# Kernel tuning notes

Measured on AMD Instinct MI355X. Metric: run time of the kernel, lower is better.

Reference implementation:

```python
import jax, jax.numpy as jnp
import numpy as np

N = 262144          # number of coordinate points
IN = 3              # coordinate dim
FF = 256            # fourier feature dim (out_features)
NFREQ = FF // 2     # 128 frequencies
H = 256             # mlp hidden width
L = 4               # hidden sine layers
OUT = 2             # Fullmodel hard-codes out_features=2 for the MLP
OMEGA0 = 30.0


def setup_inputs() -> dict:
    key = jax.random.key(0)
    ks = jax.random.split(key, 12)
    x = jax.random.normal(ks[0], (N, IN), dtype=jnp.float32)
    # Fourier encoder params (non-trainable in torch, still float inputs here)
    scales = jnp.ones((1, IN), dtype=jnp.float32)  # coordinate_scales = [1,1,1]
    B = jax.random.normal(ks[1], (IN, NFREQ), dtype=jnp.float32) * 3.0 * 10.0  # N(0,3)*10
    # SIREN first layer: uniform(-1/in, 1/in), in = FF
    W0 = jax.random.uniform(ks[2], (H, FF), dtype=jnp.float32, minval=-1.0 / FF, maxval=1.0 / FF)
    b0 = jax.random.uniform(ks[3], (H,), dtype=jnp.float32, minval=-1.0 / np.sqrt(FF), maxval=1.0 / np.sqrt(FF))
    # Hidden sine layers: uniform(-sqrt(6/in), sqrt(6/in)), in = H
    c = float(np.sqrt(6.0 / H))
    Wh = jax.random.uniform(ks[4], (L, H, H), dtype=jnp.float32, minval=-c, maxval=c)
    bh = jax.random.uniform(ks[5], (L, H), dtype=jnp.float32, minval=-1.0 / np.sqrt(H), maxval=1.0 / np.sqrt(H))
    # Final plain linear H -> OUT (default torch init, any small values fine)
    Wf = jax.random.uniform(ks[6], (OUT, H), dtype=jnp.float32, minval=-1.0 / np.sqrt(H), maxval=1.0 / np.sqrt(H))
    bf = jax.random.uniform(ks[7], (OUT,), dtype=jnp.float32, minval=-1.0 / np.sqrt(H), maxval=1.0 / np.sqrt(H))
    return {"x": x, "scales": scales, "B": B, "W0": W0, "b0": b0,
            "Wh": Wh, "bh": bh, "Wf": Wf, "bf": bf}


def reference(x, scales, B, W0, b0, Wh, bh, Wf, bf):
    # Fourier feature map: sqrt(2) * [sin(proj), cos(proj)]
    proj = (x * scales) @ B                                   # [N, NFREQ]
    sqrt2 = jnp.float32(np.sqrt(2.0))
    h = jnp.concatenate([jnp.sin(proj), jnp.cos(proj)], axis=-1) * sqrt2  # [N, FF]
    # First SIREN layer: sin(omega0 * (W x + b))
    h = jnp.sin(OMEGA0 * (h @ W0.T + b0))                     # [N, H]
    # Hidden sine layers: sin(W x + b)
    for i in range(L):
        h = jnp.sin(h @ Wh[i].T + bh[i])                      # [N, H]
    return h @ Wf.T + bf                                      # [N, OUT]
```

## Files before the change

### kernel.cpp

```cpp
#include <hip/hip_runtime.h>
#include <hip/hip_bf16.h>


typedef __attribute__((ext_vector_type(8))) short bf16x8;
typedef __attribute__((ext_vector_type(4))) float f32x4;

#define NTOTAL 262144
#define BM 64
#define HD 256
#define INV2PI 0.15915494309189535f

__device__ __forceinline__ unsigned short f2bf(float f) {
    unsigned int u = __float_as_uint(f);
    u += 0x7FFFu + ((u >> 16) & 1u);
    return (unsigned short)(u >> 16);
}

__device__ __forceinline__ unsigned int pk2(float a, float b) {
    __hip_bfloat162 h = __float22bfloat162_rn(make_float2(a, b));
    union { __hip_bfloat162 h; unsigned int u; } c;
    c.h = h;
    return c.u;
}

__device__ __forceinline__ float sin_rev(float rev) {
    return __builtin_amdgcn_sinf(__builtin_amdgcn_fractf(rev));
}

__device__ __forceinline__ int a_off(int r, int byte) {
    return r * 512 + (byte ^ ((r & 7) << 4));
}

__global__ void convert_w(const float* __restrict__ W0, const float* __restrict__ Wh,
                          const float* __restrict__ Wf, unsigned short* __restrict__ wb) {
    const int i = blockIdx.x * 256 + threadIdx.x;
    if (i < 327680) {
        const int l = i >> 16, rem = i & 65535;
        const int j = rem >> 8, k = rem & 255;
        const float v = (l == 0) ? W0[rem] * 1.41421356237309515f : Wh[i - 65536];
        const int jt = j >> 4, kt = k >> 5, q = (k >> 3) & 3, r = j & 15, t = k & 7;
        const int dst = (l << 16) + (((jt << 3) + kt) << 9) + (((q << 4) + r) << 3) + t;
        wb[dst] = f2bf(v);
    }
    if (i < 4096)
        wb[327680 + i] = (i < 512) ? f2bf(Wf[i]) : (unsigned short)0;
}

__global__ __launch_bounds__(256, 3) void siren_fused(
    const float* __restrict__ x, const float* __restrict__ scales,
    const float* __restrict__ Bm, const float* __restrict__ b0,
    const float* __restrict__ bh, const float* __restrict__ bfin,
    const unsigned short* __restrict__ wb, float* __restrict__ out) {

    __shared__ __align__(16) unsigned short A[BM * HD];

    const int tid  = threadIdx.x;
    const int lane = tid & 63;
    const int wid  = tid >> 6;
    const int row0 = blockIdx.x * BM;
    const int arow = lane & 15;
    const int q    = lane >> 4;
    const int kq   = q * 8;

    bf16x8 wfbuf[2][4];
    #pragma unroll
    for (int jt = 0; jt < 4; ++jt)
        wfbuf[0][jt] = *(const bf16x8*)(wb + (((wid * 4 + jt) << 3) << 9) + lane * 8);

    {
        const int r  = tid >> 2;
        const int c0 = (tid & 3) * 32;
        const float* xr = x + (row0 + r) * 3;
        const float x0 = xr[0] * scales[0] * INV2PI;
        const float x1 = xr[1] * scales[1] * INV2PI;
        const float x2 = xr[2] * scales[2] * INV2PI;
        #pragma unroll
        for (int cc = 0; cc < 32; cc += 8) {
            const int c = c0 + cc;
            float sv[8], cv[8];
            #pragma unroll
            for (int t = 0; t < 8; ++t) {
                const float rev = x0 * Bm[c + t] + x1 * Bm[128 + c + t] + x2 * Bm[256 + c + t];
                const float fr  = __builtin_amdgcn_fractf(rev);
                sv[t] = __builtin_amdgcn_sinf(fr);
                cv[t] = __builtin_amdgcn_cosf(fr);
            }
            uint4 us, uc;
            us.x = pk2(sv[0], sv[1]); us.y = pk2(sv[2], sv[3]);
            us.z = pk2(sv[4], sv[5]); us.w = pk2(sv[6], sv[7]);
            uc.x = pk2(cv[0], cv[1]); uc.y = pk2(cv[2], cv[3]);
            uc.z = pk2(cv[4], cv[5]); uc.w = pk2(cv[6], cv[7]);
            *(uint4*)((char*)A + a_off(r, 2 * c))         = us;
            *(uint4*)((char*)A + a_off(r, 2 * (c + 128))) = uc;
        }
    }

    #pragma unroll 1
    for (int layer = 0; layer < 5; ++layer) {
        const unsigned short* Wl = wb + (layer << 16);

        __syncthreads();

        f32x4 acc[4][4];
        #pragma unroll
        for (int a = 0; a < 4; ++a)
            #pragma unroll
            for (int b = 0; b < 4; ++b)
                acc[a][b] = (f32x4)(0.0f);

        #pragma unroll
        for (int kt = 0; kt < 8; ++kt) {
            const int cur = kt & 1, nxt = cur ^ 1;
            bf16x8 hf[4];
            #pragma unroll
            for (int rt = 0; rt < 4; ++rt)
                hf[rt] = *(const bf16x8*)((const char*)A +
                    a_off(rt * 16 + arow, kt * 64 + q * 16));
            if (kt < 7) {
                #pragma unroll
                for (int jt = 0; jt < 4; ++jt)
                    wfbuf[nxt][jt] = *(const bf16x8*)(Wl +
                        ((((wid * 4 + jt) << 3) + kt + 1) << 9) + lane * 8);
            }
            #pragma unroll
            for (int jt = 0; jt < 4; ++jt)
                #pragma unroll
                for (int rt = 0; rt < 4; ++rt)
                    acc[jt][rt] = __builtin_amdgcn_mfma_f32_16x16x32_bf16(
                        wfbuf[cur][jt], hf[rt], acc[jt][rt], 0, 0, 0);
        }

        __syncthreads();

        if (layer < 4) {
            const unsigned short* Wn = wb + ((layer + 1) << 16);
            #pragma unroll
            for (int jt = 0; jt < 4; ++jt)
                wfbuf[0][jt] = *(const bf16x8*)(Wn + (((wid * 4 + jt) << 3) << 9) + lane * 8);
        }

        const float s = (layer == 0) ? (30.0f * INV2PI) : INV2PI;
        const float* bias = (layer == 0) ? b0 : (bh + (layer - 1) * HD);
        #pragma unroll
        for (int jt = 0; jt < 4; ++jt) {
            const int jj = wid * 64 + jt * 16 + q * 4;
            float4 bv = *(const float4*)(bias + jj);
            bv.x *= s; bv.y *= s; bv.z *= s; bv.w *= s;
            #pragma unroll
            for (int rt = 0; rt < 4; ++rt) {
                const int r = rt * 16 + arow;
                const float s0 = sin_rev(fmaf(acc[jt][rt][0], s, bv.x));
                const float s1 = sin_rev(fmaf(acc[jt][rt][1], s, bv.y));
                const float s2 = sin_rev(fmaf(acc[jt][rt][2], s, bv.z));
                const float s3 = sin_rev(fmaf(acc[jt][rt][3], s, bv.w));
                uint2 val;
                val.x = pk2(s0, s1);
                val.y = pk2(s2, s3);
                *(uint2*)((char*)A + a_off(r, jj * 2)) = val;
            }
        }
    }

    __syncthreads();

    {
        const unsigned short* Wfp = wb + 327680;
        f32x4 acc = (f32x4)(0.0f);
        #pragma unroll
        for (int kt = 0; kt < 8; ++kt) {
            const bf16x8 ff = *(const bf16x8*)(Wfp + arow * HD + kt * 32 + kq);
            const bf16x8 hf = *(const bf16x8*)((const char*)A +
                a_off(wid * 16 + arow, kt * 64 + q * 16));
            acc = __builtin_amdgcn_mfma_f32_16x16x32_bf16(ff, hf, acc, 0, 0, 0);
        }
        if (q == 0) {
            const int rg = row0 + wid * 16 + arow;
            float2 o;
            o.x = acc[0] + bfin[0];
            o.y = acc[1] + bfin[1];
            *(float2*)(out + rg * 2) = o;
        }
    }
}

extern "C" void kernel_launch(void* const* d_in, const int* in_sizes, int n_in,
                              void* d_out, int out_size, void* d_ws, size_t ws_size,
                              hipStream_t stream) {
    (void)in_sizes; (void)n_in; (void)out_size; (void)ws_size;
    const float* x      = (const float*)d_in[0];
    const float* scales = (const float*)d_in[1];
    const float* Bm     = (const float*)d_in[2];
    const float* W0     = (const float*)d_in[3];
    const float* b0     = (const float*)d_in[4];
    const float* Wh     = (const float*)d_in[5];
    const float* bh     = (const float*)d_in[6];
    const float* Wf     = (const float*)d_in[7];
    const float* bf     = (const float*)d_in[8];
    unsigned short* wb  = (unsigned short*)d_ws;

    hipLaunchKernelGGL(convert_w, dim3(1280), dim3(256), 0, stream, W0, Wh, Wf, wb);
    hipLaunchKernelGGL(siren_fused, dim3(NTOTAL / BM), dim3(256), 0, stream,
                       x, scales, Bm, b0, bh, bf, wb, (float*)d_out);
}
```

Before: 202.7 us.

## Give each wave private 16-row slab and drop block-level barriers

Restructures the work split so each wave computes all 256 output features for its own 16 rows and keeps activations in registers, using a per-wave LDS slab only to transpose outputs into the next layer's fragment layout. The weight layout is reordered so k-blocks are contiguous. This removes all __syncthreads between layers. In exchange, each wave now loads the entire weight matrix per layer, quadrupling global/L2 weight traffic and lowering MFMA work per weight load.

```diff
diff --git a/kernel.cpp b/kernel.cpp
--- a/kernel.cpp
+++ b/kernel.cpp
@@ -6,7 +6,6 @@
 typedef __attribute__((ext_vector_type(4))) float f32x4;
 
 #define NTOTAL 262144
-#define BM 64
 #define HD 256
 #define INV2PI 0.15915494309189535f
 
@@ -27,10 +26,6 @@
     return __builtin_amdgcn_sinf(__builtin_amdgcn_fractf(rev));
 }
 
-__device__ __forceinline__ int a_off(int r, int byte) {
-    return r * 512 + (byte ^ ((r & 7) << 4));
-}
-
 __global__ void convert_w(const float* __restrict__ W0, const float* __restrict__ Wh,
                           const float* __restrict__ Wf, unsigned short* __restrict__ wb) {
     const int i = blockIdx.x * 256 + threadIdx.x;
@@ -39,7 +34,7 @@
         const int j = rem >> 8, k = rem & 255;
         const float v = (l == 0) ? W0[rem] * 1.41421356237309515f : Wh[i - 65536];
         const int jt = j >> 4, kt = k >> 5, q = (k >> 3) & 3, r = j & 15, t = k & 7;
-        const int dst = (l << 16) + (((jt << 3) + kt) << 9) + (((q << 4) + r) << 3) + t;
+        const int dst = (l << 16) + (((kt << 4) + jt) << 9) + (((q << 4) + r) << 3) + t;
         wb[dst] = f2bf(v);
     }
     if (i < 4096)
@@ -52,46 +47,47 @@
     const float* __restrict__ bh, const float* __restrict__ bfin,
     const unsigned short* __restrict__ wb, float* __restrict__ out) {
 
-    __shared__ __align__(16) unsigned short A[BM * HD];
+    __shared__ __align__(16) unsigned short A[4 * 16 * HD];
 
     const int tid  = threadIdx.x;
     const int lane = tid & 63;
     const int wid  = tid >> 6;
-    const int row0 = blockIdx.x * BM;
     const int arow = lane & 15;
     const int q    = lane >> 4;
-    const int kq   = q * 8;
+    const int wrow0 = blockIdx.x * 64 + wid * 16;
+    char* slab = (char*)A + wid * 8192;
+    const int xr = (arow & 7) << 4;
+    const int rb = arow * 512;
 
-    bf16x8 wfbuf[2][4];
+    bf16x8 wfb[2][4];
     #pragma unroll
-    for (int jt = 0; jt < 4; ++jt)
-        wfbuf[0][jt] = *(const bf16x8*)(wb + (((wid * 4 + jt) << 3) << 9) + lane * 8);
+    for (int jj = 0; jj < 4; ++jj)
+        wfb[0][jj] = *(const bf16x8*)(wb + (jj << 9) + lane * 8);
 
+    bf16x8 hb[8];
     {
-        const int r  = tid >> 2;
-        const int c0 = (tid & 3) * 32;
-        const float* xr = x + (row0 + r) * 3;
-        const float x0 = xr[0] * scales[0] * INV2PI;
-        const float x1 = xr[1] * scales[1] * INV2PI;
-        const float x2 = xr[2] * scales[2] * INV2PI;
+        const float* xrow = x + (wrow0 + arow) * 3;
+        const float x0 = xrow[0] * scales[0] * INV2PI;
+        const float x1 = xrow[1] * scales[1] * INV2PI;
+        const float x2 = xrow[2] * scales[2] * INV2PI;
         #pragma unroll
-        for (int cc = 0; cc < 32; cc += 8) {
-            const int c = c0 + cc;
+        for (int m = 0; m < 4; ++m) {
             float sv[8], cv[8];
             #pragma unroll
             for (int t = 0; t < 8; ++t) {
-                const float rev = x0 * Bm[c + t] + x1 * Bm[128 + c + t] + x2 * Bm[256 + c + t];
+                const int c = m * 32 + q * 8 + t;
+                const float rev = x0 * Bm[c] + x1 * Bm[128 + c] + x2 * Bm[256 + c];
                 const float fr  = __builtin_amdgcn_fractf(rev);
                 sv[t] = __builtin_amdgcn_sinf(fr);
                 cv[t] = __builtin_amdgcn_cosf(fr);
             }
-            uint4 us, uc;
-            us.x = pk2(sv[0], sv[1]); us.y = pk2(sv[2], sv[3]);
-            us.z = pk2(sv[4], sv[5]); us.w = pk2(sv[6], sv[7]);
-            uc.x = pk2(cv[0], cv[1]); uc.y = pk2(cv[2], cv[3]);
-            uc.z = pk2(cv[4], cv[5]); uc.w = pk2(cv[6], cv[7]);
-            *(uint4*)((char*)A + a_off(r, 2 * c))         = us;
-            *(uint4*)((char*)A + a_off(r, 2 * (c + 128))) = uc;
+            union { uint4 u; bf16x8 v; } cs, cc;
+            cs.u.x = pk2(sv[0], sv[1]); cs.u.y = pk2(sv[2], sv[3]);
+            cs.u.z = pk2(sv[4], sv[5]); cs.u.w = pk2(sv[6], sv[7]);
+            cc.u.x = pk2(cv[0], cv[1]); cc.u.y = pk2(cv[2], cv[3]);
+            cc.u.z = pk2(cv[4], cv[5]); cc.u.w = pk2(cv[6], cv[7]);
+            hb[m]     = cs.v;
+            hb[m + 4] = cc.v;
         }
     }
 
@@ -99,86 +95,66 @@
     for (int layer = 0; layer < 5; ++layer) {
         const unsigned short* Wl = wb + (layer << 16);
 
-        __syncthreads();
-
-        f32x4 acc[4][4];
+        f32x4 acc[16];
         #pragma unroll
-        for (int a = 0; a < 4; ++a)
-            #pragma unroll
-            for (int b = 0; b < 4; ++b)
-                acc[a][b] = (f32x4)(0.0f);
+        for (int a = 0; a < 16; ++a) acc[a] = (f32x4)(0.0f);
 
         #pragma unroll
-        for (int kt = 0; kt < 8; ++kt) {
-            const int cur = kt & 1, nxt = cur ^ 1;
-            bf16x8 hf[4];
-            #pragma unroll
-            for (int rt = 0; rt < 4; ++rt)
-                hf[rt] = *(const bf16x8*)((const char*)A +
-                    a_off(rt * 16 + arow, kt * 64 + q * 16));
-            if (kt < 7) {
+        for (int u = 0; u < 32; ++u) {
+            const int kb = u >> 2, jg = u & 3;
+            const int cur = u & 1, nxt = cur ^ 1;
+            if (u < 31) {
+                const int frag1 = (u + 1) << 2;
                 #pragma unroll
-                for (int jt = 0; jt < 4; ++jt)
-                    wfbuf[nxt][jt] = *(const bf16x8*)(Wl +
-                        ((((wid * 4 + jt) << 3) + kt + 1) << 9) + lane * 8);
+                for (int jj = 0; jj < 4; ++jj)
+                    wfb[nxt][jj] = *(const bf16x8*)(Wl + ((frag1 + jj) << 9) + lane * 8);
             }
             #pragma unroll
-            for (int jt = 0; jt < 4; ++jt)
-                #pragma unroll
-                for (int rt = 0; rt < 4; ++rt)
-                    acc[jt][rt] = __builtin_amdgcn_mfma_f32_16x16x32_bf16(
-                        wfbuf[cur][jt], hf[rt], acc[jt][rt], 0, 0, 0);
+            for (int jj = 0; jj < 4; ++jj)
+                acc[jg * 4 + jj] = __builtin_amdgcn_mfma_f32_16x16x32_bf16(
+                    wfb[cur][jj], hb[kb], acc[jg * 4 + jj], 0, 0, 0);
         }
-
-        __syncthreads();
 
         if (layer < 4) {
             const unsigned short* Wn = wb + ((layer + 1) << 16);
             #pragma unroll
-            for (int jt = 0; jt < 4; ++jt)
-                wfbuf[0][jt] = *(const bf16x8*)(Wn + (((wid * 4 + jt) << 3) << 9) + lane * 8);
+            for (int jj = 0; jj < 4; ++jj)
+                wfb[0][jj] = *(const bf16x8*)(Wn + (jj << 9) + lane * 8);
         }
 
         const float s = (layer == 0) ? (30.0f * INV2PI) : INV2PI;
         const float* bias = (layer == 0) ? b0 : (bh + (layer - 1) * HD);
         #pragma unroll
-        for (int jt = 0; jt < 4; ++jt) {
-            const int jj = wid * 64 + jt * 16 + q * 4;
-            float4 bv = *(const float4*)(bias + jj);
-            bv.x *= s; bv.y *= s; bv.z *= s; bv.w *= s;
-            #pragma unroll
-            for (int rt = 0; rt < 4; ++rt) {
-                const int r = rt * 16 + arow;
-                const float s0 = sin_rev(fmaf(acc[jt][rt][0], s, bv.x));
-                const float s1 = sin_rev(fmaf(acc[jt][rt][1], s, bv.y));
-                const float s2 = sin_rev(fmaf(acc[jt][rt][2], s, bv.z));
-                const float s3 = sin_rev(fmaf(acc[jt][rt][3], s, bv.w));
-                uint2 val;
-                val.x = pk2(s0, s1);
-                val.y = pk2(s2, s3);
-                *(uint2*)((char*)A + a_off(r, jj * 2)) = val;
-            }
+        for (int jt = 0; jt < 16; ++jt) {
+            float4 bv = *(const float4*)(bias + jt * 16 + q * 4);
+            const float e0 = sin_rev(fmaf(acc[jt][0], s, bv.x * s));
+            const float e1 = sin_rev(fmaf(acc[jt][1], s, bv.y * s));
+            const float e2 = sin_rev(fmaf(acc[jt][2], s, bv.z * s));
+            const float e3 = sin_rev(fmaf(acc[jt][3], s, bv.w * s));
+            uint2 val;
+            val.x = pk2(e0, e1);
+            val.y = pk2(e2, e3);
+            *(uint2*)(slab + rb + ((jt * 32 + q * 8) ^ xr)) = val;
         }
+
+        #pragma unroll
+        for (int kb = 0; kb < 8; ++kb)
+            hb[kb] = *(const bf16x8*)(slab + rb + ((kb * 64 + q * 16) ^ xr));
     }
-
-    __syncthreads();
 
     {
         const unsigned short* Wfp = wb + 327680;
-        f32x4 acc = (f32x4)(0.0f);
+        f32x4 accf = (f32x4)(0.0f);
         #pragma unroll
         for (int kt = 0; kt < 8; ++kt) {
-            const bf16x8 ff = *(const bf16x8*)(Wfp + arow * HD + kt * 32 + kq);
-            const bf16x8 hf = *(const bf16x8*)((const char*)A +
-                a_off(wid * 16 + arow, kt * 64 + q * 16));
-            acc = __builtin_amdgcn_mfma_f32_16x16x32_bf16(ff, hf, acc, 0, 0, 0);
+            const bf16x8 ff = *(const bf16x8*)(Wfp + arow * HD + kt * 32 + q * 8);
+            accf = __builtin_amdgcn_mfma_f32_16x16x32_bf16(ff, hb[kt], accf, 0, 0, 0);
         }
         if (q == 0) {
-            const int rg = row0 + wid * 16 + arow;
             float2 o;
-            o.x = acc[0] + bfin[0];
-            o.y = acc[1] + bfin[1];
-            *(float2*)(out + rg * 2) = o;
+            o.x = accf[0] + bfin[0];
+            o.y = accf[1] + bfin[1];
+            *(float2*)(out + (wrow0 + arow) * 2) = o;
         }
     }
 }
@@ -199,6 +175,6 @@
     unsigned short* wb  = (unsigned short*)d_ws;
 
     hipLaunchKernelGGL(convert_w, dim3(1280), dim3(256), 0, stream, W0, Wh, Wf, wb);
-    hipLaunchKernelGGL(siren_fused, dim3(NTOTAL / BM), dim3(256), 0, stream,
+    hipLaunchKernelGGL(siren_fused, dim3(NTOTAL / 64), dim3(256), 0, stream,
                        x, scales, Bm, b0, bh, bf, wb, (float*)d_out);
 }
```

New measurement: 372.6 us. 1.84x slower.
